# Optimization experiments

Measured on AMD Instinct MI355X. Metric: run time of the kernel, lower is better.

## Reference

```python
import jax, jax.numpy as jnp
import numpy as np

EMBED_DIM = 1024
NUM_HEADS = 16
HEAD_DIM = EMBED_DIM // NUM_HEADS
N_PATCHES = 220
ROPE_BASE = 10000.0
EPS = 1e-6


def rms_norm(x, g):
    # x: [..., d]
    rms = jnp.sqrt(jnp.mean(x * x, axis=-1, keepdims=True) + EPS)
    return g * (x / rms)


def apply_rope(x):
    # torchtune-style interleaved RoPE. x: [b, s, h, d]
    b, s, h, d = x.shape
    theta = 1.0 / (ROPE_BASE ** (jnp.arange(0, d, 2, dtype=jnp.float32) / d))  # [d/2]
    ang = jnp.arange(s, dtype=jnp.float32)[:, None] * theta[None, :]           # [s, d/2]
    cos = jnp.cos(ang)[None, :, None, :]
    sin = jnp.sin(ang)[None, :, None, :]
    xs = x.reshape(b, s, h, d // 2, 2)
    x0, x1 = xs[..., 0], xs[..., 1]
    out = jnp.stack([x0 * cos - x1 * sin, x1 * cos + x0 * sin], axis=-1)
    return out.reshape(b, s, h, d).astype(x.dtype)


def attention_block(x, w_qkv, w_proj, b_proj, q_gain, k_gain):
    # x: [N, S, C]; one SDPA branch (shared by spatial & temporal paths)
    N, S, C = x.shape
    H, D = NUM_HEADS, HEAD_DIM
    qkv = jnp.einsum('nsc,ec->nse', x, w_qkv).reshape(N, S, 3, H, D)
    q, k, v = qkv[:, :, 0], qkv[:, :, 1], qkv[:, :, 2]  # [N, S, H, D]
    q = apply_rope(rms_norm(q, q_gain))
    k = apply_rope(rms_norm(k, k_gain))
    scale = 1.0 / jnp.sqrt(jnp.float32(D))
    scores = jnp.einsum('nqhd,nkhd->nhqk', q, k) * scale
    attn = jax.nn.softmax(scores, axis=-1)
    out = jnp.einsum('nhqk,nkhd->nqhd', attn, v).reshape(N, S, C)
    return jnp.einsum('nsc,ec->nse', out, w_proj) + b_proj


def setup_inputs() -> dict:
    key = jax.random.key(0)
    ks = jax.random.split(key, 8)
    E = EMBED_DIM
    sd = 1.0 / np.sqrt(E)
    x = jax.random.normal(ks[0], (4, 5280, E), dtype=jnp.float32)
    w_sqkv = jax.random.uniform(ks[1], (3 * E, E), jnp.float32, -sd, sd)
    w_sproj = jax.random.uniform(ks[2], (E, E), jnp.float32, -sd, sd)
    b_sproj = jax.random.uniform(ks[3], (E,), jnp.float32, -sd, sd)
    w_tqkv = jax.random.uniform(ks[4], (3 * E, E), jnp.float32, -sd, sd)
    w_tproj = jax.random.uniform(ks[5], (E, E), jnp.float32, -sd, sd)
    b_tproj = jax.random.uniform(ks[6], (E,), jnp.float32, -sd, sd)
    g = jnp.ones((HEAD_DIM,), jnp.float32)
    return {
        'x': x,
        'w_sqkv': w_sqkv, 'w_sproj': w_sproj, 'b_sproj': b_sproj,
        'w_tqkv': w_tqkv, 'w_tproj': w_tproj, 'b_tproj': b_tproj,
        'sq_gain': g, 'sk_gain': g, 'tq_gain': g, 'tk_gain': g,
    }


def reference(x, w_sqkv, w_sproj, b_sproj, w_tqkv, w_tproj, b_tproj,
              sq_gain, sk_gain, tq_gain, tk_gain):
    B, T, C = x.shape
    P = N_PATCHES
    F = T // P
    # spatial attention per frame: (b f) p c
    xs = x.reshape(B, F, P, C).reshape(B * F, P, C)
    out_s = attention_block(xs, w_sqkv, w_sproj, b_sproj, sq_gain, sk_gain)
    # temporal attention per patch: (b p) f c
    xt = out_s.reshape(B, F, P, C).transpose(0, 2, 1, 3).reshape(B * P, F, C)
    out_t = attention_block(xt, w_tqkv, w_tproj, b_tproj, tq_gain, tk_gain)
    # (b p) f c -> b (f p) c
    out = out_t.reshape(B, P, F, C).transpose(0, 2, 1, 3).reshape(B, F * P, C)
    return out
```

## Files before the change

kernel.cpp:

```cpp
#include <hip/hip_runtime.h>

typedef _Float16 f16;
typedef _Float16 f16x8 __attribute__((ext_vector_type(8)));
typedef f16x8 f16x8a __attribute__((may_alias));
typedef float f32x4 __attribute__((ext_vector_type(4)));

#define NTOK 21120
#define MPAD 21248
#define SCALE_Q 0.18033688f

__device__ __forceinline__ void gll16(const void* g, void* l) {
  __builtin_amdgcn_global_load_lds(
      (const __attribute__((address_space(1))) unsigned int*)g,
      (__attribute__((address_space(3))) unsigned int*)l, 16, 0, 0);
}

__device__ __forceinline__ unsigned int pack2(float a, float b) {
  union { f16 h[2]; unsigned int u; } c;
  c.h[0] = (f16)a; c.h[1] = (f16)b;
  return c.u;
}
__device__ __forceinline__ unsigned short f2h(float a) {
  union { f16 h; unsigned short u; } c; c.h = (f16)a; return c.u;
}

template <int C>
__device__ __forceinline__ float dppf(float x) {
  union { float f; int i; } u, r;
  u.f = x;
  r.i = __builtin_amdgcn_update_dpp(0, u.i, C, 0xf, 0xf, true);
  return r.f;
}

__global__ __launch_bounds__(256) void cast_kernel(
    const float* __restrict__ in, unsigned short* __restrict__ out, int n4) {
  int i = blockIdx.x * 256 + threadIdx.x;
  if (i >= n4) return;
  float4 v = ((const float4*)in)[i];
  uint2 o;
  o.x = pack2(v.x, v.y);
  o.y = pack2(v.z, v.w);
  ((uint2*)out)[i] = o;
}

__global__ __launch_bounds__(256) void transpose_cast_kernel(
    const float* __restrict__ in, unsigned short* __restrict__ out) {
  __shared__ float tile[32][33];
  int bx = blockIdx.x & 31, by = blockIdx.x >> 5;
  int tx = threadIdx.x & 31, ty = threadIdx.x >> 5;
#pragma unroll
  for (int i = 0; i < 32; i += 8)
    tile[ty + i][tx] = in[(size_t)(by * 32 + ty + i) * 1024 + bx * 32 + tx];
  __syncthreads();
#pragma unroll
  for (int i = 0; i < 32; i += 8)
    out[(size_t)(bx * 32 + ty + i) * 1024 + by * 32 + tx] = f2h(tile[tx][ty + i]);
}

__global__ __launch_bounds__(256) void bias_combine_kernel(
    const float* __restrict__ w, const float* __restrict__ b, float* __restrict__ bc) {
  int e = blockIdx.x * 256 + threadIdx.x;
  if (e >= 3072) return;
  const float4* wr = (const float4*)(w + (size_t)e * 1024);
  const float4* b4 = (const float4*)b;
  float s = 0.f;
  for (int c = 0; c < 256; ++c) {
    float4 wv = wr[c], bv = b4[c];
    s += wv.x * bv.x + wv.y * bv.y + wv.z * bv.z + wv.w * bv.w;
  }
  bc[e] = s;
}

__global__ __launch_bounds__(256) void rope_table_kernel(float2* tabS, float2* tabT) {
  int t = blockIdx.x * 256 + threadIdx.x;
  const float lb = logf(10000.0f) * (1.0f / 32.0f);
  if (t < 220 * 32) {
    int s = t >> 5, i = t & 31;
    float theta = expf(-(float)i * lb);
    float ang = (float)s * theta;
    tabS[t] = make_float2(cosf(ang), sinf(ang));
  } else if (t < 220 * 32 + 24 * 32) {
    int u = t - 220 * 32;
    int s = u >> 5, i = u & 31;
    float theta = expf(-(float)i * lb);
    float ang = (float)s * theta;
    tabT[u] = make_float2(cosf(ang), sinf(ang));
  }
}

__global__ __launch_bounds__(256) void gemm_bt(
    const unsigned short* __restrict__ A, const unsigned short* __restrict__ B,
    const float* __restrict__ bias, void* __restrict__ C,
    int M, int N, int K, int outmode,
    const float2* __restrict__ tab, const float* __restrict__ gq,
    const float* __restrict__ gk, int mode) {
  __shared__ __align__(16) unsigned short sh[16384];
  unsigned short* As = sh;
  unsigned short* Bs = sh + 8192;
  const int tid = threadIdx.x;
  const int w = tid >> 6, lane = tid & 63;
  const int l15 = lane & 15, quad = lane >> 4;
  const int wr = w >> 1, wc = w & 1;

  const int ntn = N >> 7;
  const int stride = ntn << 3;
  const int g = blockIdx.x / stride, r = blockIdx.x % stride;
  const int tn = r % ntn, tm = g * 8 + r / ntn;

  f32x4 acc[4][4];
#pragma unroll
  for (int a = 0; a < 4; ++a)
#pragma unroll
    for (int b = 0; b < 4; ++b) acc[a][b] = (f32x4){0.f, 0.f, 0.f, 0.f};

  const int srow = tid >> 3;
  const int schk = tid & 7;
  const size_t arow0 = (size_t)tm * 128;
  const size_t brow0 = (size_t)tn * 128;
  const int nk = K >> 6;

  for (int kt = 0; kt < nk; ++kt) {
    __syncthreads();
    const int kb = kt << 6;
#pragma unroll
    for (int rd = 0; rd < 4; ++rd) {
      int row = rd * 32 + srow;
      int sc = (schk ^ (row & 7)) * 8;
      gll16(A + (arow0 + row) * K + kb + sc, (char*)As + rd * 4096 + tid * 16);
      gll16(B + (brow0 + row) * K + kb + sc, (char*)Bs + rd * 4096 + tid * 16);
    }
    __syncthreads();
#pragma unroll
    for (int kk = 0; kk < 2; ++kk) {
      f16x8 af[4], bf[4];
#pragma unroll
      for (int mt = 0; mt < 4; ++mt) {
        int ra = wr * 64 + mt * 16 + l15;
        af[mt] = *(const f16x8a*)((const char*)As + ra * 128 + (((kk * 4 + quad) ^ (ra & 7)) * 16));
        int rb = wc * 64 + mt * 16 + l15;
        bf[mt] = *(const f16x8a*)((const char*)Bs + rb * 128 + (((kk * 4 + quad) ^ (rb & 7)) * 16));
      }
#pragma unroll
      for (int mt = 0; mt < 4; ++mt)
#pragma unroll
        for (int nt = 0; nt < 4; ++nt)
          acc[mt][nt] = __builtin_amdgcn_mfma_f32_16x16x32_f16(af[mt], bf[nt], acc[mt][nt], 0, 0, 0);
    }
  }

  unsigned short* Cs = (unsigned short*)C;
#pragma unroll
  for (int p = 0; p < 2; ++p) {
    __syncthreads();
#pragma unroll
    for (int mi = 0; mi < 2; ++mi) {
      int mt = p * 2 + mi;
      int rl = wr * 32 + mi * 16 + quad * 4;
#pragma unroll
      for (int nt = 0; nt < 4; ++nt) {
        int cl = wc * 64 + nt * 16 + l15;
#pragma unroll
        for (int rg = 0; rg < 4; ++rg)
          sh[(rl + rg) * 136 + cl] = f2h(acc[mt][nt][rg]);
      }
    }
    __syncthreads();
#pragma unroll
    for (int c = 0; c < 4; ++c) {
      int rl = c * 16 + (tid >> 4), cx = tid & 15;
      int grow = tm * 128 + ((rl >> 5) << 6) + p * 32 + (rl & 31);
      uint4 v = *(const uint4*)&sh[rl * 136 + cx * 8];
      *(uint4*)&Cs[(size_t)grow * N + tn * 128 + cx * 8] = v;
    }
  }
}

#define FENCE() asm volatile("" ::: "memory")
#define BAR() do { FENCE(); __builtin_amdgcn_s_barrier(); FENCE(); } while (0)
#define WAITV(N) asm volatile("s_waitcnt vmcnt(" #N ")" ::: "memory")
#define LDA(sl, i) (*(const f16x8a*)(As + (sl) * 16384 + sA[i]))
#define LDB(sl, i) (*(const f16x8a*)(Bs + (sl) * 16384 + sB[i]))
#define STAGE_A(u, sl) do { \
    gll16(aS0 + (size_t)(u) * 32, As + (sl) * 16384 + tid * 16); \
    gll16(aS1 + (size_t)(u) * 32, As + (sl) * 16384 + 8192 + tid * 16); \
  } while (0)
#define STAGE_B(u, sl) do { \
    gll16(bS0 + (size_t)(u) * 32, Bs + (sl) * 16384 + tid * 16); \
    gll16(bS1 + (size_t)(u) * 32, Bs + (sl) * 16384 + 8192 + tid * 16); \
  } while (0)
#define MM16(QB, A0_, A1_, A2_, A3_, B0_, B1_, B2_, B3_) do { \
    acc[QB + 0][0] = __builtin_amdgcn_mfma_f32_16x16x32_f16(A0_, B0_, acc[QB + 0][0], 0, 0, 0); \
    acc[QB + 0][1] = __builtin_amdgcn_mfma_f32_16x16x32_f16(A0_, B1_, acc[QB + 0][1], 0, 0, 0); \
    acc[QB + 0][2] = __builtin_amdgcn_mfma_f32_16x16x32_f16(A0_, B2_, acc[QB + 0][2], 0, 0, 0); \
    acc[QB + 0][3] = __builtin_amdgcn_mfma_f32_16x16x32_f16(A0_, B3_, acc[QB + 0][3], 0, 0, 0); \
    acc[QB + 1][0] = __builtin_amdgcn_mfma_f32_16x16x32_f16(A1_, B0_, acc[QB + 1][0], 0, 0, 0); \
    acc[QB + 1][1] = __builtin_amdgcn_mfma_f32_16x16x32_f16(A1_, B1_, acc[QB + 1][1], 0, 0, 0); \
    acc[QB + 1][2] = __builtin_amdgcn_mfma_f32_16x16x32_f16(A1_, B2_, acc[QB + 1][2], 0, 0, 0); \
    acc[QB + 1][3] = __builtin_amdgcn_mfma_f32_16x16x32_f16(A1_, B3_, acc[QB + 1][3], 0, 0, 0); \
    acc[QB + 2][0] = __builtin_amdgcn_mfma_f32_16x16x32_f16(A2_, B0_, acc[QB + 2][0], 0, 0, 0); \
    acc[QB + 2][1] = __builtin_amdgcn_mfma_f32_16x16x32_f16(A2_, B1_, acc[QB + 2][1], 0, 0, 0); \
    acc[QB + 2][2] = __builtin_amdgcn_mfma_f32_16x16x32_f16(A2_, B2_, acc[QB + 2][2], 0, 0, 0); \
    acc[QB + 2][3] = __builtin_amdgcn_mfma_f32_16x16x32_f16(A2_, B3_, acc[QB + 2][3], 0, 0, 0); \
    acc[QB + 3][0] = __builtin_amdgcn_mfma_f32_16x16x32_f16(A3_, B0_, acc[QB + 3][0], 0, 0, 0); \
    acc[QB + 3][1] = __builtin_amdgcn_mfma_f32_16x16x32_f16(A3_, B1_, acc[QB + 3][1], 0, 0, 0); \
    acc[QB + 3][2] = __builtin_amdgcn_mfma_f32_16x16x32_f16(A3_, B2_, acc[QB + 3][2], 0, 0, 0); \
    acc[QB + 3][3] = __builtin_amdgcn_mfma_f32_16x16x32_f16(A3_, B3_, acc[QB + 3][3], 0, 0, 0); \
  } while (0)

__global__ __launch_bounds__(512, 2) void gemm256(
    const unsigned short* __restrict__ A, const unsigned short* __restrict__ B,
    const float* __restrict__ bias, void* __restrict__ C,
    int M, int N, int K, int outmode,
    const float2* __restrict__ tab, const float* __restrict__ gq,
    const float* __restrict__ gk, int mode) {
  extern __shared__ char smem[];
  char* As = smem;
  char* Bs = smem + 65536;
  const int tid = threadIdx.x;
  const int w = tid >> 6, lane = tid & 63;
  const int l15 = lane & 15, quad = lane >> 4;
  const int wr = w >> 2, wc = w & 3;

  const int nwg = gridDim.x;
  const int qd = nwg >> 3, rm = nwg & 7;
  const int xcd = blockIdx.x & 7, lin = blockIdx.x >> 3;
  const int wgid = (xcd < rm ? xcd * (qd + 1) : rm * (qd + 1) + (xcd - rm) * qd) + lin;
  const int ntn = N >> 8;
  const int stg = ntn << 3;
  const int g = wgid / stg, r2 = wgid % stg;
  const int tn = r2 % ntn, tm = g * 8 + r2 / ntn;

  int sA[8], sB[4];
#pragma unroll
  for (int mt = 0; mt < 8; ++mt) {
    int ra = wr * 128 + mt * 16 + l15;
    sA[mt] = ra * 64 + ((quad ^ ((ra >> 1) & 3)) << 4);
  }
#pragma unroll
  for (int nt = 0; nt < 4; ++nt) {
    int rb = wc * 64 + nt * 16 + l15;
    sB[nt] = rb * 64 + ((quad ^ ((rb >> 1) & 3)) << 4);
  }

  const int srow = tid >> 2;
  const int ssw = ((tid & 3) ^ ((tid >> 3) & 3)) << 3;
  const unsigned short* aS0 = A + (size_t)(tm * 256 + srow) * K + ssw;
  const unsigned short* aS1 = A + (size_t)(tm * 256 + 128 + srow) * K + ssw;
  const unsigned short* bS0 = B + (size_t)(tn * 256 + srow) * K + ssw;
  const unsigned short* bS1 = B + (size_t)(tn * 256 + 128 + srow) * K + ssw;

  f32x4 acc[8][4];
#pragma unroll
  for (int i = 0; i < 8; ++i)
#pragma unroll
    for (int j = 0; j < 4; ++j) acc[i][j] = (f32x4){0.f, 0.f, 0.f, 0.f};

  STAGE_A(0, 0); STAGE_B(0, 0);
  STAGE_A(1, 1); STAGE_B(1, 1);
  STAGE_A(2, 2); STAGE_B(2, 2);
  WAITV(8);
  BAR();

#pragma unroll 2
  for (int t = 0; t < 16; ++t) {
    const int s0 = (t & 1) << 1, s1 = s0 | 1, st3 = s0 ^ 3;
    const int u3 = 2 * t + 3;
    f16x8 b0, b1, b2, b3;
    b0 = LDB(s0, 0); b1 = LDB(s0, 1); b2 = LDB(s0, 2); b3 = LDB(s0, 3);
    {
      f16x8 a0 = LDA(s0, 0), a1 = LDA(s0, 1), a2 = LDA(s0, 2), a3 = LDA(s0, 3);
      if (t <= 14) STAGE_A(u3, st3);
      BAR();
      __builtin_amdgcn_s_setprio(1);
      MM16(0, a0, a1, a2, a3, b0, b1, b2, b3);
      __builtin_amdgcn_s_setprio(0);
      BAR();
    }
    {
      f16x8 a0 = LDA(s0, 4), a1 = LDA(s0, 5), a2 = LDA(s0, 6), a3 = LDA(s0, 7);
      if (t <= 14) STAGE_B(u3, st3);
      BAR();
      __builtin_amdgcn_s_setprio(1);
      MM16(4, a0, a1, a2, a3, b0, b1, b2, b3);
      __builtin_amdgcn_s_setprio(0);
      if (t <= 14) { WAITV(8); } else { WAITV(0); }
      BAR();
    }
    b0 = LDB(s1, 0); b1 = LDB(s1, 1); b2 = LDB(s1, 2); b3 = LDB(s1, 3);
    {
      f16x8 a0 = LDA(s1, 0), a1 = LDA(s1, 1), a2 = LDA(s1, 2), a3 = LDA(s1, 3);
      if (t <= 13) STAGE_A(u3 + 1, s0);
      BAR();
      __builtin_amdgcn_s_setprio(1);
      MM16(0, a0, a1, a2, a3, b0, b1, b2, b3);
      __builtin_amdgcn_s_setprio(0);
      BAR();
    }
    {
      f16x8 a0 = LDA(s1, 4), a1 = LDA(s1, 5), a2 = LDA(s1, 6), a3 = LDA(s1, 7);
      if (t <= 13) STAGE_B(u3 + 1, s0);
      BAR();
      __builtin_amdgcn_s_setprio(1);
      MM16(4, a0, a1, a2, a3, b0, b1, b2, b3);
      __builtin_amdgcn_s_setprio(0);
      if (t <= 13) { WAITV(8); } else if (t == 14) { WAITV(4); }
      BAR();
    }
  }

  BAR();
  const size_t grow0 = (size_t)tm * 256 + wr * 128;
  const int gcol0 = tn * 256 + wc * 64;

  float bl[4] = {0.f, 0.f, 0.f, 0.f};
  if (bias != nullptr) {
#pragma unroll
    for (int nt = 0; nt < 4; ++nt) bl[nt] = bias[gcol0 + nt * 16 + l15];
  }

  if (outmode == 2) {
    float* wf = (float*)(smem + w * 16384);
    const int frow = lane >> 4, fc = lane & 15;
#pragma unroll
    for (int h = 0; h < 2; ++h) {
#pragma unroll
      for (int mi = 0; mi < 4; ++mi)
#pragma unroll
        for (int nt = 0; nt < 4; ++nt)
#pragma unroll
          for (int rg = 0; rg < 4; ++rg) {
            int row = mi * 16 + quad * 4 + rg;
            int col = nt * 16 + l15;
            int c = col >> 2, lo = col & 3;
            wf[row * 64 + ((c ^ (row & 15)) << 2) + lo] = acc[h * 4 + mi][nt][rg] + bl[nt];
          }
#pragma unroll
      for (int it = 0; it < 16; ++it) {
        int row = it * 4 + frow;
        float4 v = *(const float4*)(wf + row * 64 + ((fc ^ (row & 15)) << 2));
        size_t gr = grow0 + h * 64 + row;
        if (gr < (size_t)M)
          *(float4*)((float*)C + gr * N + gcol0 + fc * 4) = v;
      }
    }
    return;
  }

  unsigned short* wh = (unsigned short*)(smem + w * 16384);
  if (outmode == 3 && tn < 8) {
    const int isQ = tn < 4;
    const float* gg = isQ ? gq : gk;
    float gv[4];
#pragma unroll
    for (int nt = 0; nt < 4; ++nt) gv[nt] = gg[nt * 16 + l15];
#pragma unroll
    for (int mt = 0; mt < 8; ++mt) {
      float v[4][4], rr[4];
#pragma unroll
      for (int rg = 0; rg < 4; ++rg) rr[rg] = 0.f;
#pragma unroll
      for (int nt = 0; nt < 4; ++nt)
#pragma unroll
        for (int rg = 0; rg < 4; ++rg) {
          float x = acc[mt][nt][rg] + bl[nt];
          v[nt][rg] = x;
          rr[rg] += x * x;
        }
#pragma unroll
      for (int rg = 0; rg < 4; ++rg) {
        float s = rr[rg];
        s += dppf<0xB1>(s);
        s += dppf<0x4E>(s);
        s += dppf<0x141>(s);
        s += dppf<0x140>(s);
        float r = rsqrtf(s * (1.0f / 64.0f) + 1e-6f);
        rr[rg] = isQ ? r * SCALE_Q : r;
      }
      int pos[4];
#pragma unroll
      for (int rg = 0; rg < 4; ++rg) {
        int grow = (int)grow0 + mt * 16 + quad * 4 + rg;
        pos[rg] = mode ? ((grow / 220) % 24) : (grow % 220);
      }
#pragma unroll
      for (int nt = 0; nt < 4; ++nt) {
        int col = nt * 16 + l15;
        int ii = nt * 8 + (l15 >> 1);
        int c = col >> 3, lo = col & 7;
#pragma unroll
        for (int rg = 0; rg < 4; ++rg) {
          float2 cs = tab[pos[rg] * 32 + ii];
          float x = v[nt][rg] * rr[rg] * gv[nt];
          float p = dppf<0xB1>(x);
          float o = (l15 & 1) ? (x * cs.x + p * cs.y) : (x * cs.x - p * cs.y);
          int row = mt * 16 + quad * 4 + rg;
          wh[row * 64 + ((c ^ (row & 7)) << 3) + lo] = f2h(o);
        }
      }
    }
  } else {
#pragma unroll
    for (int mt = 0; mt < 8; ++mt)
#pragma unroll
      for (int nt = 0; nt < 4; ++nt) {
        int col = nt * 16 + l15;
        int c = col >> 3, lo = col & 7;
#pragma unroll
        for (int rg = 0; rg < 4; ++rg) {
          int row = mt * 16 + quad * 4 + rg;
          wh[row * 64 + ((c ^ (row & 7)) << 3) + lo] = f2h(acc[mt][nt][rg] + bl[nt]);
        }
      }
  }
  {
    const int frow = lane >> 3, fch = lane & 7;
    unsigned short* C16 = (unsigned short*)C;
#pragma unroll
    for (int it = 0; it < 16; ++it) {
      int row = it * 8 + frow;
      uint4 vv = *(const uint4*)((const char*)wh + row * 128 + ((fch ^ (row & 7)) << 4));
      size_t gr = grow0 + row;
      if (gr < (size_t)M)
        *(uint4*)(C16 + gr * N + gcol0 + fch * 8) = vv;
    }
  }
}

__global__ __launch_bounds__(256) void attn_spatial(
    const unsigned short* __restrict__ qkv, unsigned short* __restrict__ aout) {
  __shared__ __align__(16) unsigned short sh[30720];
  unsigned short* Kls = sh;
  unsigned short* Vt = sh + 8192;
  unsigned short* P = sh + 22528;
  const int tid = threadIdx.x;
  const int w = tid >> 6, lane = tid & 63;
  const int l15 = lane & 15, quad = lane >> 4;
  const int n = blockIdx.x >> 4, h = blockIdx.x & 15;
  const size_t tb = (size_t)n * 220;
  const unsigned short* qbase = qkv + tb * 3072 + h * 64;

  f16x8 aq[4][2];
#pragma unroll
  for (int mt = 0; mt < 4; ++mt) {
    int row = w * 64 + mt * 16 + l15;
    if (row > 219) row = 219;
#pragma unroll
    for (int c = 0; c < 2; ++c)
      aq[mt][c] = *(const f16x8a*)(qbase + (size_t)row * 3072 + c * 32 + quad * 8);
  }
  if (tid < 220) {
    const uint4* src = (const uint4*)(qbase + (size_t)tid * 3072 + 2048);
    uint4 vv[8];
#pragma unroll
    for (int c = 0; c < 8; ++c) vv[c] = src[c];
    const unsigned short* us = (const unsigned short*)vv;
#pragma unroll
    for (int d = 0; d < 64; ++d) Vt[d * 224 + tid] = us[d];
  } else if (tid < 224) {
#pragma unroll
    for (int d = 0; d < 64; ++d) Vt[d * 224 + tid] = 0;
  }

  float lsum[4][4];
  f32x4 o[4][4];
#pragma unroll
  for (int mt = 0; mt < 4; ++mt)
#pragma unroll
    for (int rg = 0; rg < 4; ++rg) lsum[mt][rg] = 0.f;
#pragma unroll
  for (int mt = 0; mt < 4; ++mt)
#pragma unroll
    for (int nt = 0; nt < 4; ++nt) o[mt][nt] = (f32x4){0.f, 0.f, 0.f, 0.f};

  const int xr = (l15 & 3) ^ ((l15 >> 2) & 3);
  unsigned short* Pw = P + w * 2048;

  for (int half = 0; half < 2; ++half) {
    const int k0 = half * 128;
    const int nslot = half ? 736 : 1024;
#pragma unroll
    for (int k = 0; k < 4; ++k) {
      int slot = k * 256 + tid;
      if (slot < nslot) {
        int rl = slot >> 3, c = slot & 7;
        gll16(qbase + (size_t)(k0 + rl) * 3072 + 1024 + ((c ^ (rl & 7)) * 8),
              (char*)Kls + k * 4096 + w * 1024);
      }
    }
    __syncthreads();
    const int nci = half ? 3 : 4;
    for (int ci = 0; ci < nci; ++ci) {
      const int cig = half * 4 + ci;
      f16x8 bk[2][2];
#pragma unroll
      for (int ct = 0; ct < 2; ++ct) {
        int rl = ci * 32 + ct * 16 + l15;
#pragma unroll
        for (int c = 0; c < 2; ++c)
          bk[ct][c] = *(const f16x8a*)((const char*)Kls + rl * 128 + (((quad + 4 * c) ^ (rl & 7)) * 16));
      }
      f32x4 sc[4][2];
#pragma unroll
      for (int mt = 0; mt < 4; ++mt)
#pragma unroll
        for (int ct = 0; ct < 2; ++ct) {
          f32x4 z = (f32x4){0.f, 0.f, 0.f, 0.f};
          z = __builtin_amdgcn_mfma_f32_16x16x32_f16(aq[mt][0], bk[ct][0], z, 0, 0, 0);
          sc[mt][ct] = __builtin_amdgcn_mfma_f32_16x16x32_f16(aq[mt][1], bk[ct][1], z, 0, 0, 0);
        }
      const int okk = (cig * 32 + 16 + l15) < 220;
#pragma unroll
      for (int mt = 0; mt < 4; ++mt)
#pragma unroll
        for (int rg = 0; rg < 4; ++rg) {
          float p0 = exp2f(sc[mt][0][rg]);
          float p1 = okk ? exp2f(sc[mt][1][rg]) : 0.0f;
          lsum[mt][rg] += p0 + p1;
          int xw = quad ^ rg;
          unsigned short* pb = Pw + (mt * 16 + quad * 4 + rg) * 32;
          pb[(((l15 >> 3) ^ xw) * 8) + (l15 & 7)] = f2h(p0);
          pb[(((2 + (l15 >> 3)) ^ xw) * 8) + (l15 & 7)] = f2h(p1);
        }
      __asm__ volatile("s_waitcnt lgkmcnt(0)" ::: "memory");
      f16x8 ap[4], bv[4];
#pragma unroll
      for (int mt = 0; mt < 4; ++mt)
        ap[mt] = *(const f16x8a*)((const char*)Pw + (mt * 16 + l15) * 64 + (quad ^ xr) * 16);
#pragma unroll
      for (int nt = 0; nt < 4; ++nt)
        bv[nt] = *(const f16x8a*)((const char*)Vt + (nt * 16 + l15) * 448 + cig * 64 + quad * 16);
#pragma unroll
      for (int mt = 0; mt < 4; ++mt)
#pragma unroll
        for (int nt = 0; nt < 4; ++nt)
          o[mt][nt] = __builtin_amdgcn_mfma_f32_16x16x32_f16(ap[mt], bv[nt], o[mt][nt], 0, 0, 0);
    }
    __syncthreads();
  }

#pragma unroll
  for (int mt = 0; mt < 4; ++mt)
#pragma unroll
    for (int rg = 0; rg < 4; ++rg) {
      float l = lsum[mt][rg];
      l += __shfl_xor(l, 1);
      l += __shfl_xor(l, 2);
      l += __shfl_xor(l, 4);
      l += __shfl_xor(l, 8);
      int s = w * 64 + mt * 16 + quad * 4 + rg;
      if (s < 220) {
        float inv = 1.0f / l;
        unsigned short* dst = aout + (tb + s) * 1024 + h * 64;
#pragma unroll
        for (int nt = 0; nt < 4; ++nt) dst[nt * 16 + l15] = f2h(o[mt][nt][rg] * inv);
      }
    }
}

__global__ __launch_bounds__(256) void attn_temporal(
    const unsigned short* __restrict__ qkv, unsigned short* __restrict__ aout) {
  __shared__ __align__(16) unsigned short sh[14336];
  const int tid = threadIdx.x;
  const int w = tid >> 6, lane = tid & 63;
  const int l15 = lane & 15, quad = lane >> 4;
  const int b = blockIdx.x / 880;
  const int rem = blockIdx.x % 880;
  const int p = rem >> 2, hq = rem & 3;
  const int h = hq * 4 + w;
  unsigned short* Vtw = sh + w * 2560;
  unsigned short* Pw = sh + 10240 + w * 1024;
  const unsigned short* base = qkv + ((size_t)(b * 24) * 220 + p) * 3072 + h * 64;
  const size_t fs = (size_t)220 * 3072;

  {
    int r = lane >> 1, hf = lane & 1;
    if (r < 24) {
      const uint4* src = (const uint4*)(base + r * fs + 2048 + hf * 32);
      uint4 vv[4];
#pragma unroll
      for (int c = 0; c < 4; ++c) vv[c] = src[c];
      const unsigned short* us = (const unsigned short*)vv;
#pragma unroll
      for (int j = 0; j < 32; ++j) Vtw[(hf * 32 + j) * 40 + r] = us[j];
    } else {
#pragma unroll
      for (int j = 0; j < 32; ++j) Vtw[(hf * 32 + j) * 40 + r] = 0;
    }
  }
  f16x8 aq[2][2], bk[2][2];
#pragma unroll
  for (int mt = 0; mt < 2; ++mt) {
    int row = mt * 16 + l15;
    if (row > 23) row = 23;
#pragma unroll
    for (int c = 0; c < 2; ++c)
      aq[mt][c] = *(const f16x8a*)(base + row * fs + c * 32 + quad * 8);
  }
#pragma unroll
  for (int ct = 0; ct < 2; ++ct) {
    int row = ct * 16 + l15;
    if (row > 23) row = 23;
#pragma unroll
    for (int c = 0; c < 2; ++c)
      bk[ct][c] = *(const f16x8a*)(base + row * fs + 1024 + c * 32 + quad * 8);
  }
  f32x4 sc[2][2];
#pragma unroll
  for (int mt = 0; mt < 2; ++mt)
#pragma unroll
    for (int ct = 0; ct < 2; ++ct) {
      f32x4 z = (f32x4){0.f, 0.f, 0.f, 0.f};
      z = __builtin_amdgcn_mfma_f32_16x16x32_f16(aq[mt][0], bk[ct][0], z, 0, 0, 0);
      sc[mt][ct] = __builtin_amdgcn_mfma_f32_16x16x32_f16(aq[mt][1], bk[ct][1], z, 0, 0, 0);
    }
  const int xr = (l15 & 3) ^ ((l15 >> 2) & 3);
  const int okk = l15 < 8;
  float lr[2][4];
#pragma unroll
  for (int mt = 0; mt < 2; ++mt)
#pragma unroll
    for (int rg = 0; rg < 4; ++rg) {
      float p0 = exp2f(sc[mt][0][rg]);
      float p1 = okk ? exp2f(sc[mt][1][rg]) : 0.0f;
      float rs = p0 + p1;
      rs += __shfl_xor(rs, 1);
      rs += __shfl_xor(rs, 2);
      rs += __shfl_xor(rs, 4);
      rs += __shfl_xor(rs, 8);
      lr[mt][rg] = rs;
      int xw = quad ^ rg;
      unsigned short* pb = Pw + (mt * 16 + quad * 4 + rg) * 32;
      pb[(((l15 >> 3) ^ xw) * 8) + (l15 & 7)] = f2h(p0);
      pb[(((2 + (l15 >> 3)) ^ xw) * 8) + (l15 & 7)] = f2h(p1);
    }
  __asm__ volatile("s_waitcnt lgkmcnt(0)" ::: "memory");
  f16x8 ap[2], bv[4];
#pragma unroll
  for (int mt = 0; mt < 2; ++mt)
    ap[mt] = *(const f16x8a*)((const char*)Pw + (mt * 16 + l15) * 64 + (quad ^ xr) * 16);
#pragma unroll
  for (int nt = 0; nt < 4; ++nt)
    bv[nt] = *(const f16x8a*)((const char*)Vtw + (nt * 16 + l15) * 80 + quad * 16);
  f32x4 o[2][4];
#pragma unroll
  for (int mt = 0; mt < 2; ++mt)
#pragma unroll
    for (int nt = 0; nt < 4; ++nt) {
      f32x4 z = (f32x4){0.f, 0.f, 0.f, 0.f};
      o[mt][nt] = __builtin_amdgcn_mfma_f32_16x16x32_f16(ap[mt], bv[nt], z, 0, 0, 0);
    }
#pragma unroll
  for (int mt = 0; mt < 2; ++mt)
#pragma unroll
    for (int rg = 0; rg < 4; ++rg) {
      int s = mt * 16 + quad * 4 + rg;
      if (s < 24) {
        float inv = 1.0f / lr[mt][rg];
        unsigned short* dst = aout + ((size_t)(b * 24 + s) * 220 + p) * 1024 + h * 64;
#pragma unroll
        for (int nt = 0; nt < 4; ++nt) dst[nt * 16 + l15] = f2h(o[mt][nt][rg] * inv);
      }
    }
}

extern "C" void kernel_launch(void* const* d_in, const int* in_sizes, int n_in,
                              void* d_out, int out_size, void* d_ws, size_t ws_size,
                              hipStream_t stream) {
  (void)in_sizes; (void)n_in; (void)out_size; (void)ws_size;
  const float* x = (const float*)d_in[0];
  const float* wsqkv = (const float*)d_in[1];
  const float* wsproj = (const float*)d_in[2];
  const float* bsproj = (const float*)d_in[3];
  const float* wtqkv = (const float*)d_in[4];
  const float* wtproj = (const float*)d_in[5];
  const float* btproj = (const float*)d_in[6];
  const float* sqg = (const float*)d_in[7];
  const float* skg = (const float*)d_in[8];
  const float* tqg = (const float*)d_in[9];
  const float* tkg = (const float*)d_in[10];

  static bool attr_done = false;
  if (!attr_done) {
    hipFuncSetAttribute(reinterpret_cast<const void*>(gemm256),
                        hipFuncAttributeMaxDynamicSharedMemorySize, 131072);
    attr_done = true;
  }

  char* ws = (char*)d_ws;
  size_t off = 0;
  auto alloc = [&](size_t bytes) {
    char* ptr = ws + off;
    off += (bytes + 255) & ~(size_t)255;
    return ptr;
  };
  unsigned short* xb = (unsigned short*)alloc((size_t)MPAD * 1024 * 2);
  unsigned short* qkvb = (unsigned short*)alloc((size_t)NTOK * 3072 * 2);
  unsigned short* aoutb = (unsigned short*)alloc((size_t)MPAD * 1024 * 2);
  unsigned short* wsqkvb = (unsigned short*)alloc((size_t)3072 * 1024 * 2);
  unsigned short* wsprojTb = (unsigned short*)alloc((size_t)1024 * 1024 * 2);
  unsigned short* wtqkvb = (unsigned short*)alloc((size_t)3072 * 1024 * 2);
  unsigned short* wtprojb = (unsigned short*)alloc((size_t)1024 * 1024 * 2);
  unsigned short* wcb = (unsigned short*)alloc((size_t)3072 * 1024 * 2);
  float* bcb = (float*)alloc(3072 * 4);
  float2* tabS = (float2*)alloc(220 * 32 * 8);
  float2* tabT = (float2*)alloc(24 * 32 * 8);

  hipMemsetAsync(xb + (size_t)NTOK * 1024, 0, (size_t)(MPAD - NTOK) * 1024 * 2, stream);
  hipMemsetAsync(aoutb + (size_t)NTOK * 1024, 0, (size_t)(MPAD - NTOK) * 1024 * 2, stream);

  dim3 blk(256);
  cast_kernel<<<21120, blk, 0, stream>>>(x, xb, 5406720);
  cast_kernel<<<3072, blk, 0, stream>>>(wsqkv, wsqkvb, 786432);
  cast_kernel<<<3072, blk, 0, stream>>>(wtqkv, wtqkvb, 786432);
  cast_kernel<<<1024, blk, 0, stream>>>(wtproj, wtprojb, 262144);
  transpose_cast_kernel<<<1024, blk, 0, stream>>>(wsproj, wsprojTb);
  bias_combine_kernel<<<12, blk, 0, stream>>>(wtqkv, bsproj, bcb);
  rope_table_kernel<<<31, blk, 0, stream>>>(tabS, tabT);

  gemm_bt<<<dim3(24 * 8), blk, 0, stream>>>(wtqkvb, wsprojTb, nullptr, wcb, 3072, 1024, 1024, 0,
                                            nullptr, nullptr, nullptr, 0);

  dim3 blk512(512);
  gemm256<<<dim3(83 * 12), blk512, 131072, stream>>>(xb, wsqkvb, nullptr, qkvb, NTOK, 3072, 1024, 3,
                                                     tabS, sqg, skg, 0);
  attn_spatial<<<dim3(1536), blk, 0, stream>>>(qkvb, aoutb);
  gemm256<<<dim3(83 * 12), blk512, 131072, stream>>>(aoutb, wcb, bcb, qkvb, NTOK, 3072, 1024, 3,
                                                     tabT, tqg, tkg, 1);
  attn_temporal<<<dim3(3520), blk, 0, stream>>>(qkvb, aoutb);
  gemm256<<<dim3(83 * 4), blk512, 131072, stream>>>(aoutb, wtprojb, btproj, (float*)d_out,
                                                    NTOK, 1024, 1024, 2,
                                                    nullptr, nullptr, nullptr, 0);
}
```

Before: 760.0 us.

## Widen GEMM K-tile to 64 with asymmetric triple/double LDS buffering

Reworks the main GEMM256 loop to load K=64 chunks per stage, with three LDS slots for A and two for B and an 8-way XOR swizzle. This halves the number of barrier rounds per K and gives A a deeper prefetch. LDS per block grows to 160KB, which likely drops residency from two workgroups per CU to one and reduces latency hiding.

```diff
diff --git a/kernel.cpp b/kernel.cpp
--- a/kernel.cpp
+++ b/kernel.cpp
@@ -178,15 +178,17 @@
 #define FENCE() asm volatile("" ::: "memory")
 #define BAR() do { FENCE(); __builtin_amdgcn_s_barrier(); FENCE(); } while (0)
 #define WAITV(N) asm volatile("s_waitcnt vmcnt(" #N ")" ::: "memory")
-#define LDA(sl, i) (*(const f16x8a*)(As + (sl) * 16384 + sA[i]))
-#define LDB(sl, i) (*(const f16x8a*)(Bs + (sl) * 16384 + sB[i]))
-#define STAGE_A(u, sl) do { \
-    gll16(aS0 + (size_t)(u) * 32, As + (sl) * 16384 + tid * 16); \
-    gll16(aS1 + (size_t)(u) * 32, As + (sl) * 16384 + 8192 + tid * 16); \
+#define ASLOT(T) (((T) % 3) * 32768)
+#define BSLOT(T) (98304 + ((T) & 1) * 32768)
+#define LDAf(T, mt, kk) (*(const f16x8a*)(smem + ASLOT(T) + wrOff + (mt) * 2048 + (aoff ^ ((kk) << 6))))
+#define LDBf(T, nt, kk) (*(const f16x8a*)(smem + BSLOT(T) + bcOff + (nt) * 2048 + (aoff ^ ((kk) << 6))))
+#define STAGE_A2(T, h) do { \
+    gll16(aSp + (size_t)((h) * 128) * K + (T) * 64, smem + ASLOT(T) + (h) * 16384 + tid * 16); \
+    gll16(aSp + (size_t)((h) * 128 + 64) * K + (T) * 64, smem + ASLOT(T) + (h) * 16384 + 8192 + tid * 16); \
   } while (0)
-#define STAGE_B(u, sl) do { \
-    gll16(bS0 + (size_t)(u) * 32, Bs + (sl) * 16384 + tid * 16); \
-    gll16(bS1 + (size_t)(u) * 32, Bs + (sl) * 16384 + 8192 + tid * 16); \
+#define STAGE_B2(T, h) do { \
+    gll16(bSp + (size_t)((h) * 128) * K + (T) * 64, smem + BSLOT(T) + (h) * 16384 + tid * 16); \
+    gll16(bSp + (size_t)((h) * 128 + 64) * K + (T) * 64, smem + BSLOT(T) + (h) * 16384 + 8192 + tid * 16); \
   } while (0)
 #define MM16(QB, A0_, A1_, A2_, A3_, B0_, B1_, B2_, B3_) do { \
     acc[QB + 0][0] = __builtin_amdgcn_mfma_f32_16x16x32_f16(A0_, B0_, acc[QB + 0][0], 0, 0, 0); \
@@ -214,8 +216,6 @@
     const float2* __restrict__ tab, const float* __restrict__ gq,
     const float* __restrict__ gk, int mode) {
   extern __shared__ char smem[];
-  char* As = smem;
-  char* Bs = smem + 65536;
   const int tid = threadIdx.x;
   const int w = tid >> 6, lane = tid & 63;
   const int l15 = lane & 15, quad = lane >> 4;
@@ -230,24 +230,13 @@
   const int g = wgid / stg, r2 = wgid % stg;
   const int tn = r2 % ntn, tm = g * 8 + r2 / ntn;
 
-  int sA[8], sB[4];
-#pragma unroll
-  for (int mt = 0; mt < 8; ++mt) {
-    int ra = wr * 128 + mt * 16 + l15;
-    sA[mt] = ra * 64 + ((quad ^ ((ra >> 1) & 3)) << 4);
-  }
-#pragma unroll
-  for (int nt = 0; nt < 4; ++nt) {
-    int rb = wc * 64 + nt * 16 + l15;
-    sB[nt] = rb * 64 + ((quad ^ ((rb >> 1) & 3)) << 4);
-  }
-
-  const int srow = tid >> 2;
-  const int ssw = ((tid & 3) ^ ((tid >> 3) & 3)) << 3;
-  const unsigned short* aS0 = A + (size_t)(tm * 256 + srow) * K + ssw;
-  const unsigned short* aS1 = A + (size_t)(tm * 256 + 128 + srow) * K + ssw;
-  const unsigned short* bS0 = B + (size_t)(tn * 256 + srow) * K + ssw;
-  const unsigned short* bS1 = B + (size_t)(tn * 256 + 128 + srow) * K + ssw;
+  const int wrOff = wr * 16384;
+  const int bcOff = (wc >> 1) * 16384 + (wc & 1) * 8192;
+  const int aoff = l15 * 128 + ((quad ^ (l15 & 7)) << 4);
+
+  const int sc = ((tid & 7) ^ ((tid >> 3) & 7)) * 8;
+  const unsigned short* aSp = A + (size_t)(tm * 256 + (tid >> 3)) * K + sc;
+  const unsigned short* bSp = B + (size_t)(tn * 256 + (tid >> 3)) * K + sc;
 
   f32x4 acc[8][4];
 #pragma unroll
@@ -255,57 +244,46 @@
 #pragma unroll
     for (int j = 0; j < 4; ++j) acc[i][j] = (f32x4){0.f, 0.f, 0.f, 0.f};
 
-  STAGE_A(0, 0); STAGE_B(0, 0);
-  STAGE_A(1, 1); STAGE_B(1, 1);
-  STAGE_A(2, 2); STAGE_B(2, 2);
-  WAITV(8);
+  STAGE_A2(0, 0); STAGE_A2(0, 1);
+  STAGE_B2(0, 0); STAGE_B2(0, 1);
+  STAGE_A2(1, 0); STAGE_A2(1, 1);
+  WAITV(4);
   BAR();
 
-#pragma unroll 2
+#pragma unroll
   for (int t = 0; t < 16; ++t) {
-    const int s0 = (t & 1) << 1, s1 = s0 | 1, st3 = s0 ^ 3;
-    const int u3 = 2 * t + 3;
-    f16x8 b0, b1, b2, b3;
-    b0 = LDB(s0, 0); b1 = LDB(s0, 1); b2 = LDB(s0, 2); b3 = LDB(s0, 3);
-    {
-      f16x8 a0 = LDA(s0, 0), a1 = LDA(s0, 1), a2 = LDA(s0, 2), a3 = LDA(s0, 3);
-      if (t <= 14) STAGE_A(u3, st3);
-      BAR();
-      __builtin_amdgcn_s_setprio(1);
-      MM16(0, a0, a1, a2, a3, b0, b1, b2, b3);
-      __builtin_amdgcn_s_setprio(0);
-      BAR();
-    }
-    {
-      f16x8 a0 = LDA(s0, 4), a1 = LDA(s0, 5), a2 = LDA(s0, 6), a3 = LDA(s0, 7);
-      if (t <= 14) STAGE_B(u3, st3);
-      BAR();
-      __builtin_amdgcn_s_setprio(1);
-      MM16(4, a0, a1, a2, a3, b0, b1, b2, b3);
-      __builtin_amdgcn_s_setprio(0);
-      if (t <= 14) { WAITV(8); } else { WAITV(0); }
-      BAR();
-    }
-    b0 = LDB(s1, 0); b1 = LDB(s1, 1); b2 = LDB(s1, 2); b3 = LDB(s1, 3);
-    {
-      f16x8 a0 = LDA(s1, 0), a1 = LDA(s1, 1), a2 = LDA(s1, 2), a3 = LDA(s1, 3);
-      if (t <= 13) STAGE_A(u3 + 1, s0);
-      BAR();
-      __builtin_amdgcn_s_setprio(1);
-      MM16(0, a0, a1, a2, a3, b0, b1, b2, b3);
-      __builtin_amdgcn_s_setprio(0);
-      BAR();
-    }
-    {
-      f16x8 a0 = LDA(s1, 4), a1 = LDA(s1, 5), a2 = LDA(s1, 6), a3 = LDA(s1, 7);
-      if (t <= 13) STAGE_B(u3 + 1, s0);
-      BAR();
-      __builtin_amdgcn_s_setprio(1);
-      MM16(4, a0, a1, a2, a3, b0, b1, b2, b3);
-      __builtin_amdgcn_s_setprio(0);
-      if (t <= 13) { WAITV(8); } else if (t == 14) { WAITV(4); }
-      BAR();
-    }
+    f16x8 a0, a1, a2, a3, b0, b1, b2, b3;
+    b0 = LDBf(t, 0, 0); b1 = LDBf(t, 1, 0); b2 = LDBf(t, 2, 0); b3 = LDBf(t, 3, 0);
+    a0 = LDAf(t, 0, 0); a1 = LDAf(t, 1, 0); a2 = LDAf(t, 2, 0); a3 = LDAf(t, 3, 0);
+    if (t <= 14) STAGE_B2(t + 1, 0);
+    BAR();
+    __builtin_amdgcn_s_setprio(1);
+    MM16(0, a0, a1, a2, a3, b0, b1, b2, b3);
+    __builtin_amdgcn_s_setprio(0);
+    BAR();
+    a0 = LDAf(t, 4, 0); a1 = LDAf(t, 5, 0); a2 = LDAf(t, 6, 0); a3 = LDAf(t, 7, 0);
+    if (t <= 14) STAGE_B2(t + 1, 1);
+    BAR();
+    __builtin_amdgcn_s_setprio(1);
+    MM16(4, a0, a1, a2, a3, b0, b1, b2, b3);
+    __builtin_amdgcn_s_setprio(0);
+    BAR();
+    b0 = LDBf(t, 0, 1); b1 = LDBf(t, 1, 1); b2 = LDBf(t, 2, 1); b3 = LDBf(t, 3, 1);
+    a0 = LDAf(t, 0, 1); a1 = LDAf(t, 1, 1); a2 = LDAf(t, 2, 1); a3 = LDAf(t, 3, 1);
+    if (t <= 13) STAGE_A2(t + 2, 0);
+    BAR();
+    __builtin_amdgcn_s_setprio(1);
+    MM16(0, a0, a1, a2, a3, b0, b1, b2, b3);
+    __builtin_amdgcn_s_setprio(0);
+    BAR();
+    a0 = LDAf(t, 4, 1); a1 = LDAf(t, 5, 1); a2 = LDAf(t, 6, 1); a3 = LDAf(t, 7, 1);
+    if (t <= 13) STAGE_A2(t + 2, 1);
+    BAR();
+    __builtin_amdgcn_s_setprio(1);
+    MM16(4, a0, a1, a2, a3, b0, b1, b2, b3);
+    __builtin_amdgcn_s_setprio(0);
+    if (t <= 13) { WAITV(4); } else if (t == 14) { WAITV(0); }
+    BAR();
   }
 
   BAR();
@@ -682,7 +660,7 @@
   static bool attr_done = false;
   if (!attr_done) {
     hipFuncSetAttribute(reinterpret_cast<const void*>(gemm256),
-                        hipFuncAttributeMaxDynamicSharedMemorySize, 131072);
+                        hipFuncAttributeMaxDynamicSharedMemorySize, 163840);
     attr_done = true;
   }
 
@@ -721,13 +699,13 @@
                                             nullptr, nullptr, nullptr, 0);
 
   dim3 blk512(512);
-  gemm256<<<dim3(83 * 12), blk512, 131072, stream>>>(xb, wsqkvb, nullptr, qkvb, NTOK, 3072, 1024, 3,
+  gemm256<<<dim3(83 * 12), blk512, 163840, stream>>>(xb, wsqkvb, nullptr, qkvb, NTOK, 3072, 1024, 3,
                                                      tabS, sqg, skg, 0);
   attn_spatial<<<dim3(1536), blk, 0, stream>>>(qkvb, aoutb);
-  gemm256<<<dim3(83 * 12), blk512, 131072, stream>>>(aoutb, wcb, bcb, qkvb, NTOK, 3072, 1024, 3,
+  gemm256<<<dim3(83 * 12), blk512, 163840, stream>>>(aoutb, wcb, bcb, qkvb, NTOK, 3072, 1024, 3,
                                                      tabT, tqg, tkg, 1);
   attn_temporal<<<dim3(3520), blk, 0, stream>>>(qkvb, aoutb);
-  gemm256<<<dim3(83 * 4), blk512, 131072, stream>>>(aoutb, wtprojb, btproj, (float*)d_out,
+  gemm256<<<dim3(83 * 4), blk512, 163840, stream>>>(aoutb, wtprojb, btproj, (float*)d_out,
                                                     NTOK, 1024, 1024, 2,
                                                     nullptr, nullptr, nullptr, 0);
 }
```

Result: faster. 714.4 us (-6.0%).
